# Performance work log

Hardware: AMD Instinct MI355X
Metric: run time of the kernel (lower is better)

The kernel has to match this reference:

```python
import jax, jax.numpy as jnp
import numpy as np

DEPTH = 3  # truncation depth of the signature (init kwarg)


def _restricted_exp(v, depth):
    """Tensor-algebra exponential of an increment v: (N, C).

    Returns a tuple of flattened levels [(N, C), (N, C^2), ..., (N, C^depth)]
    where level k is v^{(x)k} / k!.
    """
    n = v.shape[0]
    levels = [v]
    for k in range(2, depth + 1):
        nxt = (levels[-1][:, :, None] * v[:, None, :]).reshape(n, -1) / k
        levels.append(nxt)
    return tuple(levels)


def _chen_mult(a, b, depth):
    """Truncated tensor-algebra product (Chen's relation).

    c_k = a_k + b_k + sum_{i+j=k, i,j>=1} a_i (x) b_j, levels flattened to (N, C^k).
    """
    n = a[0].shape[0]
    out = []
    for k in range(depth):
        term = a[k] + b[k]
        for i in range(k):
            term = term + (a[i][:, :, None] * b[k - 1 - i][:, None, :]).reshape(n, -1)
        out.append(term)
    return tuple(out)


def _signature(path, depth):
    # path: (N, L, C). Signature of the piecewise-linear path from increments.
    inc = path[:, 1:, :] - path[:, :-1, :]          # (N, L-1, C)
    inc = jnp.moveaxis(inc, 1, 0)                   # (L-1, N, C) for scan
    init = _restricted_exp(inc[0], depth)

    def step(carry, v):
        return _chen_mult(carry, _restricted_exp(v, depth), depth), None

    final, _ = jax.lax.scan(jax.checkpoint(step), init, inc[1:])
    # concat levels -> (N, C + C^2 + ... + C^depth)
    return jnp.concatenate(final, axis=-1)


def setup_inputs() -> dict:
    key = jax.random.key(0)
    path = jax.random.normal(key, (32, 128, 48), dtype=jnp.float32)
    return {"path": path}


def reference(path):
    return _signature(path, DEPTH)
```

## Files before the change

### kernel.cpp

```cpp
#include <hip/hip_runtime.h>


#define N_BATCH 32
#define LPATH   128
#define T_STEPS 127
#define C       48
#define C2      2304
#define C3      110592
#define OUT_PER_N (C + C2 + C3)
#define PATH_PER_N (LPATH * C)
#define GROUPS 27
#define RSLOT 36
#define LDS_FLOATS 6912

typedef float f32x2 __attribute__((ext_vector_type(2)));

__global__ __launch_bounds__(256, 2) void sig_fused(const float* __restrict__ path,
                                                    float* __restrict__ out) {
    __shared__ float lds[LDS_FLOATS];

    int bid = blockIdx.x;
    int n = bid / GROUPS;
    int g = bid - n * GROUPS;
    int tid = threadIdx.x;
    int q = tid >> 6;
    int lane = tid & 63;

    const float* __restrict__ pb = path + n * PATH_PER_N;

    int U = g * 64 + lane;
    int i = U / 36;
    int rr = U - i * 36;
    int jg = rr / 6;
    int kc = rr - jg * 6;

    int T0 = q * 32;

    const float* gk = pb + T0 * C + kc * 8;
    float4 A0 = *(const float4*)(gk + 0 * C);
    float4 A1 = *(const float4*)(gk + 0 * C + 4);
    float4 B0 = *(const float4*)(gk + 1 * C);
    float4 B1 = *(const float4*)(gk + 1 * C + 4);
    float4 C0 = *(const float4*)(gk + 2 * C);
    float4 C1 = *(const float4*)(gk + 2 * C + 4);
    float4 D0 = *(const float4*)(gk + 3 * C);
    float4 D1 = *(const float4*)(gk + 3 * C + 4);
    gk += 4 * C;

    {
        const float4* p4 = (const float4*)pb;
        float4* v4 = (float4*)lds;
        #pragma unroll
        for (int c = 0; c < 6; ++c) {
            int idx = tid + 256 * c;
            if (idx < (T_STEPS * C) / 4) {
                float4 a = p4[idx];
                float4 b = p4[idx + C / 4];
                v4[idx] = make_float4(b.x - a.x, b.y - a.y, b.z - a.z, b.w - a.w);
            }
        }
    }
    if (g == 0 && tid < C)
        out[(long)n * OUT_PER_N + tid] = pb[(LPATH - 1) * C + tid] - pb[tid];
    __syncthreads();

    float Pi = pb[T0 * C + i] - pb[i];
    float a2[8];
    f32x2 s3[8][4];
    #pragma unroll
    for (int jj = 0; jj < 8; ++jj) {
        a2[jj] = 0.f;
        #pragma unroll
        for (int p = 0; p < 4; ++p) s3[jj][p] = (f32x2){0.f, 0.f};
    }

    const float* ldsJ = lds + T0 * C + jg * 8;
    const float* ldsI = lds + T0 * C + i;

#define KSTEP(O0, O1, N0, N1, REL, DOLOAD) do {                         \
        float  vi_ = ldsI[(REL) * C];                                   \
        float4 vj0 = *(const float4*)(ldsJ + (REL) * C);                \
        float4 vj1 = *(const float4*)(ldsJ + (REL) * C + 4);            \
        f32x2 kk0 = {N0.x - O0.x, N0.y - O0.y};                         \
        f32x2 kk1 = {N0.z - O0.z, N0.w - O0.w};                         \
        f32x2 kk2 = {N1.x - O1.x, N1.y - O1.y};                         \
        f32x2 kk3 = {N1.z - O1.z, N1.w - O1.w};                         \
        if (DOLOAD) {                                                   \
            O0 = *(const float4*)(gk + (REL) * C);                      \
            O1 = *(const float4*)(gk + (REL) * C + 4);                  \
        }                                                               \
        float G = Pi + 0.5f * vi_;                                      \
        float R = 0.5f * Pi + (1.0f / 6.0f) * vi_;                      \
        Pi += vi_;                                                      \
        f32x2 RG = {R, G};                                              \
        float vja[8] = {vj0.x, vj0.y, vj0.z, vj0.w,                     \
                        vj1.x, vj1.y, vj1.z, vj1.w};                    \
        _Pragma("unroll")                                               \
        for (int jj = 0; jj < 8; ++jj) {                                \
            f32x2 vjp = {vja[jj], vja[jj]};                             \
            f32x2 aap = {a2[jj], a2[jj]};                               \
            f32x2 t2v = __builtin_elementwise_fma(RG, vjp, aap);        \
            a2[jj] = t2v.y;                                             \
            f32x2 bb = {t2v.x, t2v.x};                                  \
            s3[jj][0] = __builtin_elementwise_fma(bb, kk0, s3[jj][0]);  \
            s3[jj][1] = __builtin_elementwise_fma(bb, kk1, s3[jj][1]);  \
            s3[jj][2] = __builtin_elementwise_fma(bb, kk2, s3[jj][2]);  \
            s3[jj][3] = __builtin_elementwise_fma(bb, kk3, s3[jj][3]);  \
        }                                                               \
    } while (0)

    int NB = (q == 3) ? 7 : 8;
    for (int b = 0; b < NB; ++b) {
        KSTEP(A0, A1, B0, B1, 0, 1);
        KSTEP(B0, B1, C0, C1, 1, 1);
        KSTEP(C0, C1, D0, D1, 2, 1);
        KSTEP(D0, D1, A0, A1, 3, 1);
        ldsJ += 4 * C; ldsI += 4 * C; gk += 4 * C;
    }
    if (q == 3) {
        KSTEP(A0, A1, B0, B1, 0, 0);
        KSTEP(B0, B1, C0, C1, 1, 0);
        KSTEP(C0, C1, D0, D1, 2, 0);
    }
#undef KSTEP

    float4 W10, W11, W20, W21, W30, W31;
    if (q == 3) {
        float4 p32a = *(const float4*)(pb + 32 * C + kc * 8);
        float4 p32b = *(const float4*)(pb + 32 * C + kc * 8 + 4);
        float4 p64a = *(const float4*)(pb + 64 * C + kc * 8);
        float4 p64b = *(const float4*)(pb + 64 * C + kc * 8 + 4);
        float4 p96a = *(const float4*)(pb + 96 * C + kc * 8);
        float4 p96b = *(const float4*)(pb + 96 * C + kc * 8 + 4);
        float4 pEa  = *(const float4*)(pb + 127 * C + kc * 8);
        float4 pEb  = *(const float4*)(pb + 127 * C + kc * 8 + 4);
        W10 = make_float4(p64a.x - p32a.x, p64a.y - p32a.y, p64a.z - p32a.z, p64a.w - p32a.w);
        W11 = make_float4(p64b.x - p32b.x, p64b.y - p32b.y, p64b.z - p32b.z, p64b.w - p32b.w);
        W20 = make_float4(p96a.x - p64a.x, p96a.y - p64a.y, p96a.z - p64a.z, p96a.w - p64a.w);
        W21 = make_float4(p96b.x - p64b.x, p96b.y - p64b.y, p96b.z - p64b.z, p96b.w - p64b.w);
        W30 = make_float4(pEa.x - p96a.x, pEa.y - p96a.y, pEa.z - p96a.z, pEa.w - p96a.w);
        W31 = make_float4(pEb.x - p96b.x, pEb.y - p96b.y, pEb.z - p96b.z, pEb.w - p96b.w);
    }

    __syncthreads();

    long obase = (long)n * OUT_PER_N + C;
    #pragma unroll
    for (int r = 0; r < 2; ++r) {
        if (r) __syncthreads();
        if (q < 3) {
            float* dst = lds + (q * RSLOT) * 64 + lane;
            #pragma unroll
            for (int jjr = 0; jjr < 4; ++jjr) {
                int jj = r * 4 + jjr;
                dst[(jjr * 8 + 0) * 64] = s3[jj][0][0];
                dst[(jjr * 8 + 1) * 64] = s3[jj][0][1];
                dst[(jjr * 8 + 2) * 64] = s3[jj][1][0];
                dst[(jjr * 8 + 3) * 64] = s3[jj][1][1];
                dst[(jjr * 8 + 4) * 64] = s3[jj][2][0];
                dst[(jjr * 8 + 5) * 64] = s3[jj][2][1];
                dst[(jjr * 8 + 6) * 64] = s3[jj][3][0];
                dst[(jjr * 8 + 7) * 64] = s3[jj][3][1];
                dst[(32 + jjr) * 64]    = a2[jj];
            }
        }
        __syncthreads();
        if (q == 3) {
            #pragma unroll
            for (int jjr = 0; jjr < 4; ++jjr) {
                int jj = r * 4 + jjr;
                const float* s0 = lds + (0 * RSLOT) * 64 + lane;
                const float* s1 = lds + (1 * RSLOT) * 64 + lane;
                const float* s2 = lds + (2 * RSLOT) * 64 + lane;
                float a2q0 = s0[(32 + jjr) * 64];
                float a2q1 = s1[(32 + jjr) * 64];
                float a2q2 = s2[(32 + jjr) * 64];
                float pre1 = a2q0;
                float pre2 = a2q0 + a2q1;
                float pre3 = pre2 + a2q2;
                float acc[8];
                #pragma unroll
                for (int c = 0; c < 8; ++c) {
                    int sl = (jjr * 8 + c) * 64;
                    acc[c] = s0[sl] + s1[sl] + s2[sl];
                }
                acc[0] += s3[jj][0][0] + pre1 * W10.x + pre2 * W20.x + pre3 * W30.x;
                acc[1] += s3[jj][0][1] + pre1 * W10.y + pre2 * W20.y + pre3 * W30.y;
                acc[2] += s3[jj][1][0] + pre1 * W10.z + pre2 * W20.z + pre3 * W30.z;
                acc[3] += s3[jj][1][1] + pre1 * W10.w + pre2 * W20.w + pre3 * W30.w;
                acc[4] += s3[jj][2][0] + pre1 * W11.x + pre2 * W21.x + pre3 * W31.x;
                acc[5] += s3[jj][2][1] + pre1 * W11.y + pre2 * W21.y + pre3 * W31.y;
                acc[6] += s3[jj][3][0] + pre1 * W11.z + pre2 * W21.z + pre3 * W31.z;
                acc[7] += s3[jj][3][1] + pre1 * W11.w + pre2 * W21.w + pre3 * W31.w;

                float* dst = out + obase + C2 + (long)(i * C + jg * 8 + jj) * C + kc * 8;
                *(float4*)(dst)     = make_float4(acc[0], acc[1], acc[2], acc[3]);
                *(float4*)(dst + 4) = make_float4(acc[4], acc[5], acc[6], acc[7]);
                if (kc == 0)
                    out[obase + i * C + jg * 8 + jj] = pre3 + a2[jj];
            }
        }
    }
}

extern "C" void kernel_launch(void* const* d_in, const int* in_sizes, int n_in,
                              void* d_out, int out_size, void* d_ws, size_t ws_size,
                              hipStream_t stream) {
    const float* path = (const float*)d_in[0];
    float* out = (float*)d_out;
    (void)d_ws; (void)ws_size;

    sig_fused<<<N_BATCH * GROUPS, 256, 0, stream>>>(path, out);
}
```

Before: 76.09 us.

## Spread final cross-wave reduction across all four waves via full LDS staging

Instead of having only wave 3 read partials from the other three waves in two LDS rounds and compute all outputs, every wave now writes its full partial state to a larger LDS buffer and each wave reduces and stores two of the eight output rows. This removes the serialized epilogue on a single wave and one barrier round. It also forces the main time loop to stay rolled, probably to limit register pressure. The cost is a larger LDS footprint (about 72 KB per block), which may reduce blocks per CU, and every wave now loads the path endpoints.

```diff
diff --git a/kernel.cpp b/kernel.cpp
--- a/kernel.cpp
+++ b/kernel.cpp
@@ -10,8 +10,8 @@
 #define OUT_PER_N (C + C2 + C3)
 #define PATH_PER_N (LPATH * C)
 #define GROUPS 27
-#define RSLOT 36
-#define LDS_FLOATS 6912
+#define RSLOT 72
+#define LDS_FLOATS 18432
 
 typedef float f32x2 __attribute__((ext_vector_type(2)));
 
@@ -110,6 +110,7 @@
     } while (0)
 
     int NB = (q == 3) ? 7 : 8;
+    #pragma unroll 1
     for (int b = 0; b < NB; ++b) {
         KSTEP(A0, A1, B0, B1, 0, 1);
         KSTEP(B0, B1, C0, C1, 1, 1);
@@ -125,7 +126,7 @@
 #undef KSTEP
 
     float4 W10, W11, W20, W21, W30, W31;
-    if (q == 3) {
+    {
         float4 p32a = *(const float4*)(pb + 32 * C + kc * 8);
         float4 p32b = *(const float4*)(pb + 32 * C + kc * 8 + 4);
         float4 p64a = *(const float4*)(pb + 64 * C + kc * 8);
@@ -144,61 +145,59 @@
 
     __syncthreads();
 
+    {
+        float* dst = lds + (q * RSLOT) * 64 + lane;
+        #pragma unroll
+        for (int jj = 0; jj < 8; ++jj) {
+            dst[(jj * 8 + 0) * 64] = s3[jj][0][0];
+            dst[(jj * 8 + 1) * 64] = s3[jj][0][1];
+            dst[(jj * 8 + 2) * 64] = s3[jj][1][0];
+            dst[(jj * 8 + 3) * 64] = s3[jj][1][1];
+            dst[(jj * 8 + 4) * 64] = s3[jj][2][0];
+            dst[(jj * 8 + 5) * 64] = s3[jj][2][1];
+            dst[(jj * 8 + 6) * 64] = s3[jj][3][0];
+            dst[(jj * 8 + 7) * 64] = s3[jj][3][1];
+            dst[(64 + jj) * 64]    = a2[jj];
+        }
+    }
+    __syncthreads();
+
     long obase = (long)n * OUT_PER_N + C;
-    #pragma unroll
-    for (int r = 0; r < 2; ++r) {
-        if (r) __syncthreads();
-        if (q < 3) {
-            float* dst = lds + (q * RSLOT) * 64 + lane;
+    {
+        const float* s0 = lds + (0 * RSLOT) * 64 + lane;
+        const float* s1 = lds + (1 * RSLOT) * 64 + lane;
+        const float* s2 = lds + (2 * RSLOT) * 64 + lane;
+        const float* s3l = lds + (3 * RSLOT) * 64 + lane;
+        #pragma unroll
+        for (int m = 0; m < 2; ++m) {
+            int jj = 4 * m + q;
+            float a2q0 = s0[(64 + jj) * 64];
+            float a2q1 = s1[(64 + jj) * 64];
+            float a2q2 = s2[(64 + jj) * 64];
+            float a2q3 = s3l[(64 + jj) * 64];
+            float pre1 = a2q0;
+            float pre2 = a2q0 + a2q1;
+            float pre3 = pre2 + a2q2;
+            float acc[8];
             #pragma unroll
-            for (int jjr = 0; jjr < 4; ++jjr) {
-                int jj = r * 4 + jjr;
-                dst[(jjr * 8 + 0) * 64] = s3[jj][0][0];
-                dst[(jjr * 8 + 1) * 64] = s3[jj][0][1];
-                dst[(jjr * 8 + 2) * 64] = s3[jj][1][0];
-                dst[(jjr * 8 + 3) * 64] = s3[jj][1][1];
-                dst[(jjr * 8 + 4) * 64] = s3[jj][2][0];
-                dst[(jjr * 8 + 5) * 64] = s3[jj][2][1];
-                dst[(jjr * 8 + 6) * 64] = s3[jj][3][0];
-                dst[(jjr * 8 + 7) * 64] = s3[jj][3][1];
-                dst[(32 + jjr) * 64]    = a2[jj];
+            for (int c = 0; c < 8; ++c) {
+                int sl = (jj * 8 + c) * 64;
+                acc[c] = s0[sl] + s1[sl] + s2[sl];
             }
-        }
-        __syncthreads();
-        if (q == 3) {
-            #pragma unroll
-            for (int jjr = 0; jjr < 4; ++jjr) {
-                int jj = r * 4 + jjr;
-                const float* s0 = lds + (0 * RSLOT) * 64 + lane;
-                const float* s1 = lds + (1 * RSLOT) * 64 + lane;
-                const float* s2 = lds + (2 * RSLOT) * 64 + lane;
-                float a2q0 = s0[(32 + jjr) * 64];
-                float a2q1 = s1[(32 + jjr) * 64];
-                float a2q2 = s2[(32 + jjr) * 64];
-                float pre1 = a2q0;
-                float pre2 = a2q0 + a2q1;
-                float pre3 = pre2 + a2q2;
-                float acc[8];
-                #pragma unroll
-                for (int c = 0; c < 8; ++c) {
-                    int sl = (jjr * 8 + c) * 64;
-                    acc[c] = s0[sl] + s1[sl] + s2[sl];
-                }
-                acc[0] += s3[jj][0][0] + pre1 * W10.x + pre2 * W20.x + pre3 * W30.x;
-                acc[1] += s3[jj][0][1] + pre1 * W10.y + pre2 * W20.y + pre3 * W30.y;
-                acc[2] += s3[jj][1][0] + pre1 * W10.z + pre2 * W20.z + pre3 * W30.z;
-                acc[3] += s3[jj][1][1] + pre1 * W10.w + pre2 * W20.w + pre3 * W30.w;
-                acc[4] += s3[jj][2][0] + pre1 * W11.x + pre2 * W21.x + pre3 * W31.x;
-                acc[5] += s3[jj][2][1] + pre1 * W11.y + pre2 * W21.y + pre3 * W31.y;
-                acc[6] += s3[jj][3][0] + pre1 * W11.z + pre2 * W21.z + pre3 * W31.z;
-                acc[7] += s3[jj][3][1] + pre1 * W11.w + pre2 * W21.w + pre3 * W31.w;
-
-                float* dst = out + obase + C2 + (long)(i * C + jg * 8 + jj) * C + kc * 8;
-                *(float4*)(dst)     = make_float4(acc[0], acc[1], acc[2], acc[3]);
-                *(float4*)(dst + 4) = make_float4(acc[4], acc[5], acc[6], acc[7]);
-                if (kc == 0)
-                    out[obase + i * C + jg * 8 + jj] = pre3 + a2[jj];
-            }
+            acc[0] += s3l[(jj * 8 + 0) * 64] + pre1 * W10.x + pre2 * W20.x + pre3 * W30.x;
+            acc[1] += s3l[(jj * 8 + 1) * 64] + pre1 * W10.y + pre2 * W20.y + pre3 * W30.y;
+            acc[2] += s3l[(jj * 8 + 2) * 64] + pre1 * W10.z + pre2 * W20.z + pre3 * W30.z;
+            acc[3] += s3l[(jj * 8 + 3) * 64] + pre1 * W10.w + pre2 * W20.w + pre3 * W30.w;
+            acc[4] += s3l[(jj * 8 + 4) * 64] + pre1 * W11.x + pre2 * W21.x + pre3 * W31.x;
+            acc[5] += s3l[(jj * 8 + 5) * 64] + pre1 * W11.y + pre2 * W21.y + pre3 * W31.y;
+            acc[6] += s3l[(jj * 8 + 6) * 64] + pre1 * W11.z + pre2 * W21.z + pre3 * W31.z;
+            acc[7] += s3l[(jj * 8 + 7) * 64] + pre1 * W11.w + pre2 * W21.w + pre3 * W31.w;
+
+            float* dstg = out + obase + C2 + (long)(i * C + jg * 8 + jj) * C + kc * 8;
+            *(float4*)(dstg)     = make_float4(acc[0], acc[1], acc[2], acc[3]);
+            *(float4*)(dstg + 4) = make_float4(acc[4], acc[5], acc[6], acc[7]);
+            if (kc == 0)
+                out[obase + i * C + jg * 8 + jj] = pre3 + a2q3;
         }
     }
 }
```

Result: slower. 77.73 us (+2.2%).
